# Performance work log

Hardware: AMD Instinct MI355X
Metric: run time of the kernel (lower is better)

The kernel has to match this reference:

```python
import jax, jax.numpy as jnp
import numpy as np

N_HEAD = 16

def setup_inputs() -> dict:
    key = jax.random.key(0)
    ks = jax.random.split(key, 5)
    C = 1024
    s = 1.0 / np.sqrt(C)
    x = jax.random.normal(ks[0], (2, 2048, C), dtype=jnp.float32)
    wq = jax.random.normal(ks[1], (C, C), dtype=jnp.float32) * s
    wk = jax.random.normal(ks[2], (C, C), dtype=jnp.float32) * s
    wv = jax.random.normal(ks[3], (C, C), dtype=jnp.float32) * s
    wp = jax.random.normal(ks[4], (C, C), dtype=jnp.float32) * s
    z = jnp.zeros((C,), dtype=jnp.float32)
    return {"x": x, "wq": wq, "bq": z, "wk": wk, "bk": z,
            "wv": wv, "bv": z, "wp": wp, "bp": z}

def reference(x, wq, bq, wk, bk, wv, bv, wp, bp):
    B, T, C = x.shape
    H = N_HEAD
    D = C // H
    # projections: weights stored as (in, out) -> x @ w + b
    q = (x @ wq + bq).reshape(B, T, H, D).transpose(0, 2, 1, 3)  # [B,H,T,D]
    k = (x @ wk + bk).reshape(B, T, H, D).transpose(0, 2, 1, 3)
    v = (x @ wv + bv).reshape(B, T, H, D).transpose(0, 2, 1, 3)
    att = jnp.einsum('bhqd,bhkd->bhqk', q, k) / jnp.sqrt(jnp.float32(D))
    causal = jnp.tril(jnp.ones((T, T), dtype=bool))
    att = jnp.where(causal[None, None], att, -jnp.inf)
    att = jax.nn.softmax(att, axis=-1)
    out = jnp.einsum('bhqk,bhkd->bhqd', att, v)  # [B,H,T,D]
    out = out.transpose(0, 2, 1, 3).reshape(B, T, C)
    return out @ wp + bp
```

## Files before the change

### kernel.cpp

```cpp
#include <hip/hip_runtime.h>
#include <hip/hip_bf16.h>
#include <stdint.h>


typedef __attribute__((ext_vector_type(8)))  short bf16x8;
typedef __attribute__((ext_vector_type(4)))  float f32x4;
typedef __attribute__((ext_vector_type(16))) float f32x16;
typedef __attribute__((ext_vector_type(4)))  short short4v;

#define MFMA16(a,b,c) __builtin_amdgcn_mfma_f32_16x16x32_bf16(a,b,c,0,0,0)
#define MFMA32(a,b,c) __builtin_amdgcn_mfma_f32_32x32x16_bf16(a,b,c,0,0,0)

__device__ __forceinline__ unsigned short f2bfu(float f){
  union { __hip_bfloat16 h; unsigned short u; } cv;
  cv.h = __float2bfloat16(f);
  return cv.u;
}

__device__ __forceinline__ unsigned cvtpk(float a, float b){
  unsigned r;
  asm("v_cvt_pk_bf16_f32 %0, %1, %2" : "=v"(r) : "v"(a), "v"(b));
  return r;
}

__device__ __forceinline__ void permswap(unsigned &x, unsigned &y){
  asm volatile("v_permlane32_swap_b32 %0, %1" : "+v"(x), "+v"(y));
}

__device__ __forceinline__ void async16(const void* g, void* s){
  __builtin_amdgcn_global_load_lds((const __attribute__((address_space(1))) void*)g,
                                   (__attribute__((address_space(3))) void*)s, 16, 0, 0);
}

__global__ __launch_bounds__(256)
void prep_k(const float* __restrict__ x, unsigned short* __restrict__ xb,
            const float* __restrict__ wq, const float* __restrict__ wk,
            const float* __restrict__ wv, const float* __restrict__ wp,
            unsigned short* __restrict__ wqkvT, unsigned short* __restrict__ wpT)
{
  __shared__ float t[32][33];
  const int bx = blockIdx.x;
  const int tid = threadIdx.x;
  if (bx < 4096) {
    const int i = bx * 256 + tid;
    const float4 v = ((const float4*)x)[i];
    short4v o;
    o.x = (short)f2bfu(v.x); o.y = (short)f2bfu(v.y);
    o.z = (short)f2bfu(v.z); o.w = (short)f2bfu(v.w);
    ((short4v*)xb)[i] = o;
    return;
  }
  const int b = bx - 4096;
  const int wsel = b >> 10;
  const float* W = (wsel == 0) ? wq : (wsel == 1) ? wk : (wsel == 2) ? wv : wp;
  unsigned short* Wt = (wsel == 3) ? wpT : wqkvT + (size_t)wsel * 1024 * 1024;
  const int bc = ((b & 1023) & 31) * 32;
  const int br = ((b & 1023) >> 5) * 32;
  const int tx = tid & 31, ty = tid >> 5;
  #pragma unroll
  for (int i = 0; i < 32; i += 8)
    t[ty + i][tx] = W[(size_t)(br + ty + i) * 1024 + bc + tx];
  __syncthreads();
  #pragma unroll
  for (int i = 0; i < 32; i += 8)
    Wt[(size_t)(bc + ty + i) * 1024 + br + tx] = f2bfu(t[tx][ty + i]);
}

template<int MODE>
__global__ __launch_bounds__(256)
void gemm_bt(const unsigned short* __restrict__ A, const unsigned short* __restrict__ Bt,
             const float* __restrict__ b0, const float* __restrict__ b1, const float* __restrict__ b2,
             unsigned short* __restrict__ Qo, unsigned short* __restrict__ Ko,
             unsigned short* __restrict__ Vo, float* __restrict__ Fo, int N)
{
  constexpr int K = 1024;
  __shared__ unsigned short As[2][128 * 32];
  __shared__ unsigned short Bs[2][128 * 32];
  const int tid = threadIdx.x;
  const int lane = tid & 63;
  const int w = tid >> 6;
  const int l15 = lane & 15, lhi = lane >> 4;
  const int row0 = blockIdx.y * 128;
  const int col0 = blockIdx.x * 128;
  const int wr = (w >> 1) * 64;
  const int wc = (w & 1) * 64;

  f32x4 acc[4][4];
  #pragma unroll
  for (int i = 0; i < 4; i++)
    #pragma unroll
    for (int j = 0; j < 4; j++) acc[i][j] = 0.0f;

  const int srow = lane >> 2;
  const int scol = (lane & 3) * 8;
  const unsigned short* Ab = A  + (size_t)(row0 + w * 32 + srow) * K + scol;
  const unsigned short* Bb = Bt + (size_t)(col0 + w * 32 + srow) * K + scol;
  const int wofs = (w * 32) * 32;

  auto stageg = [&](int k0, int buf) {
    async16(Ab + k0,          &As[buf][wofs]);
    async16(Ab + k0 + 16 * K, &As[buf][wofs + 16 * 32]);
    async16(Bb + k0,          &Bs[buf][wofs]);
    async16(Bb + k0 + 16 * K, &Bs[buf][wofs + 16 * 32]);
  };

  stageg(0, 0);
  __syncthreads();
  int cur = 0;
  for (int k0 = 0; k0 < K; k0 += 32) {
    if (k0 + 32 < K) stageg(k0 + 32, cur ^ 1);
    bf16x8 af[4], bfv[4];
    #pragma unroll
    for (int i = 0; i < 4; i++) {
      af[i]  = *(const bf16x8*)&As[cur][(wr + i * 16 + l15) * 32 + lhi * 8];
      bfv[i] = *(const bf16x8*)&Bs[cur][(wc + i * 16 + l15) * 32 + lhi * 8];
    }
    __builtin_amdgcn_s_setprio(1);
    #pragma unroll
    for (int i = 0; i < 4; i++)
      #pragma unroll
      for (int j = 0; j < 4; j++)
        acc[i][j] = MFMA16(af[i], bfv[j], acc[i][j]);
    __builtin_amdgcn_s_setprio(0);
    __syncthreads();
    cur ^= 1;
  }

  #pragma unroll
  for (int j = 0; j < 4; j++) {
    const int n = col0 + wc + j * 16 + l15;
    if constexpr (MODE == 0) {
      const int which = n >> 10;
      const int cn = n & 1023;
      const float bias = (which == 0 ? b0[cn] : which == 1 ? b1[cn] : b2[cn]);
      const int h = cn >> 6, d = cn & 63;
      if (which == 2) {
        #pragma unroll
        for (int i = 0; i < 4; i++) {
          const int m = row0 + wr + i * 16 + lhi * 4;
          const int b_ = m >> 11, t = m & 2047;
          uint2 pk;
          pk.x = cvtpk(acc[i][j][0] + bias, acc[i][j][1] + bias);
          pk.y = cvtpk(acc[i][j][2] + bias, acc[i][j][3] + bias);
          *(uint2*)(Vo + (((size_t)(b_ * 16 + h) * 64 + d) * 2048 + t)) = pk;
        }
      } else {
        unsigned short* dst = (which == 0 ? Qo : Ko);
        const float sc = (which == 0 ? 0.125f * 1.44269504f : 1.0f);
        #pragma unroll
        for (int i = 0; i < 4; i++)
          #pragma unroll
          for (int r = 0; r < 4; r++) {
            const int m = row0 + wr + i * 16 + lhi * 4 + r;
            const int b_ = m >> 11, t = m & 2047;
            dst[(((size_t)(b_ * 16 + h) * 2048 + t) * 64) + d] =
                f2bfu((acc[i][j][r] + bias) * sc);
          }
      }
    } else {
      const float bias = b0[n];
      #pragma unroll
      for (int i = 0; i < 4; i++)
        #pragma unroll
        for (int r = 0; r < 4; r++) {
          const int m = row0 + wr + i * 16 + lhi * 4 + r;
          Fo[(size_t)m * N + n] = acc[i][j][r] + bias;
        }
    }
  }
}


__global__ __launch_bounds__(256, 1)
void attn_k(const unsigned short* __restrict__ Q, const unsigned short* __restrict__ Kg,
            const unsigned short* __restrict__ VT, unsigned short* __restrict__ O)
{
  __shared__ unsigned short Ks[2][64 * 64];
  __shared__ unsigned short Vs[2][64 * 64];
  const int flat = blockIdx.y * 8 + blockIdx.x;
  const int u = (flat & 7) * 32 + (flat >> 3);
  const int bx = u & 7, bh = u >> 3;
  const int b_ = bh >> 4, h = bh & 15;
  const int tid = threadIdx.x, lane = tid & 63, w = tid >> 6;
  const int r0 = lane & 31, hi5 = lane >> 5;
  const int p  = bx * 4 + w;
  const int pB = 63 - p;
  const int q0A = p * 32, q0B = pB * 32;
  const int jmA = p >> 1, jmB = pB >> 1;
  const int jmax = (63 - bx * 4) >> 1;

  const unsigned short* Kbh  = Kg + (size_t)bh * (2048 * 64);
  const unsigned short* VTbh = VT + (size_t)bh * (64 * 2048);

  bf16x8 qfA[4], qfB[4];
  {
    const unsigned short* QA = Q + ((size_t)bh * 2048 + q0A + r0) * 64 + hi5 * 8;
    const unsigned short* QB = Q + ((size_t)bh * 2048 + q0B + r0) * 64 + hi5 * 8;
    #pragma unroll
    for (int s = 0; s < 4; s++) {
      qfA[s] = *(const bf16x8*)(QA + s * 16);
      qfB[s] = *(const bf16x8*)(QB + s * 16);
    }
  }

  f32x16 oA[2], oB[2];
  #pragma unroll
  for (int d = 0; d < 2; d++) { oA[d] = 0.0f; oB[d] = 0.0f; }
  float mA = -1e30f, lA = 0.0f, mB = -1e30f, lB = 0.0f;

  int fragoff[4];
  #pragma unroll
  for (int t = 0; t < 4; t++)
    fragoff[t] = (r0 * 128 + t * 32 + hi5 * 16) ^ ((r0 & 7) << 4);

  const int srow = w * 8 + (lane >> 3);
  const int cole = (((lane & 7) ^ (lane >> 3)) << 3);
  const unsigned short* Ksrc = Kbh + (size_t)srow * 64 + cole;
  const unsigned short* Vsrc = VTbh + (size_t)srow * 2048 + cole;

  auto stage = [&](int kv0, int buf) {
    unsigned short* kb = &Ks[buf][w * 512];
    unsigned short* vb = &Vs[buf][w * 512];
    #pragma unroll
    for (int it = 0; it < 2; ++it) {
      async16(Ksrc + (size_t)(kv0 + it * 32) * 64, kb + it * 2048);
      async16(Vsrc + (size_t)(it * 32) * 2048 + kv0, vb + it * 2048);
    }
  };

  const unsigned short* Ksb;
  const unsigned short* Vsb;

  auto member = [&](f32x16 (&oT)[2], const bf16x8 (&qf)[4],
                    float& mrun, float& lrun, int q0, int kv0, bool mask) {
    f32x16 s0 = 0.0f, s1 = 0.0f;
    __builtin_amdgcn_s_setprio(1);
    #pragma unroll
    for (int t = 0; t < 4; t++) {
      const bf16x8 ka = *(const bf16x8*)((const char*)Ksb + fragoff[t]);
      const bf16x8 kb = *(const bf16x8*)((const char*)Ksb + fragoff[t] + 4096);
      s0 = MFMA32(ka, qf[t], s0);
      s1 = MFMA32(kb, qf[t], s1);
    }
    __builtin_amdgcn_s_setprio(0);

    const int q = q0 + r0;
    if (mask) {
      #pragma unroll
      for (int r = 0; r < 16; r++) {
        const int kvr = kv0 + (r & 3) + 8 * (r >> 2) + 4 * hi5;
        if (kvr      > q) s0[r] = -1e30f;
        if (kvr + 32 > q) s1[r] = -1e30f;
      }
    }

    float pm = fmaxf(s0[0], s1[0]);
    #pragma unroll
    for (int r = 1; r < 16; r++) pm = fmaxf(pm, fmaxf(s0[r], s1[r]));
    pm = fmaxf(pm, __shfl_xor(pm, 32, 64));

    if (__any((int)(pm > mrun + 8.0f))) {
      const float mnew = fmaxf(mrun, pm);
      const float sc = exp2f(mrun - mnew);
      mrun = mnew; lrun *= sc;
      oT[0] *= sc; oT[1] *= sc;
    }

    float p0[16], p1[16];
    float rs = 0.0f;
    #pragma unroll
    for (int r = 0; r < 16; r++) {
      p0[r] = exp2f(s0[r] - mrun);
      p1[r] = exp2f(s1[r] - mrun);
      rs += p0[r] + p1[r];
    }
    rs += __shfl_xor(rs, 32, 64);
    lrun += rs;

    bf16x8 pb[4];
    #pragma unroll
    for (int sub = 0; sub < 2; sub++) {
      {
        unsigned a = cvtpk(p0[sub*8+0], p0[sub*8+1]);
        unsigned b = cvtpk(p0[sub*8+2], p0[sub*8+3]);
        unsigned c = cvtpk(p0[sub*8+4], p0[sub*8+5]);
        unsigned d = cvtpk(p0[sub*8+6], p0[sub*8+7]);
        permswap(a, c); permswap(b, d);
        union { unsigned u[4]; bf16x8 hv; } wv_;
        wv_.u[0] = a; wv_.u[1] = b; wv_.u[2] = c; wv_.u[3] = d;
        pb[sub] = wv_.hv;
      }
      {
        unsigned a = cvtpk(p1[sub*8+0], p1[sub*8+1]);
        unsigned b = cvtpk(p1[sub*8+2], p1[sub*8+3]);
        unsigned c = cvtpk(p1[sub*8+4], p1[sub*8+5]);
        unsigned d = cvtpk(p1[sub*8+6], p1[sub*8+7]);
        permswap(a, c); permswap(b, d);
        union { unsigned u[4]; bf16x8 hv; } wv_;
        wv_.u[0] = a; wv_.u[1] = b; wv_.u[2] = c; wv_.u[3] = d;
        pb[2 + sub] = wv_.hv;
      }
    }

    __builtin_amdgcn_s_setprio(1);
    #pragma unroll
    for (int t = 0; t < 4; t++) {
      const bf16x8 va = *(const bf16x8*)((const char*)Vsb + fragoff[t]);
      const bf16x8 vb = *(const bf16x8*)((const char*)Vsb + fragoff[t] + 4096);
      oT[0] = MFMA32(va, pb[t], oT[0]);
      oT[1] = MFMA32(vb, pb[t], oT[1]);
    }
    __builtin_amdgcn_s_setprio(0);
  };

  stage(0, 0);
  __syncthreads();

  int cur = 0;
  for (int j = 0; j <= jmax; ++j) {
    if (j < jmax) stage((j + 1) * 64, cur ^ 1);
    Ksb = &Ks[cur][0];
    Vsb = &Vs[cur][0];
    const int kv0 = j * 64;
    if (j <= jmB) member(oB, qfB, mB, lB, q0B, kv0, j == jmB);
    if (j <= jmA) member(oA, qfA, mA, lA, q0A, kv0, j == jmA);
    __syncthreads();
    cur ^= 1;
  }

  auto emit = [&](f32x16 (&oT)[2], float lr, int q0) {
    const float linv = 1.0f / lr;
    const int q = q0 + r0;
    unsigned short* obase = O + ((size_t)b_ * 2048 + q) * 1024 + h * 64 + hi5 * 4;
    #pragma unroll
    for (int dh = 0; dh < 2; dh++)
      #pragma unroll
      for (int g = 0; g < 4; g++) {
        uint2 pk;
        pk.x = cvtpk(oT[dh][4*g]   * linv, oT[dh][4*g+1] * linv);
        pk.y = cvtpk(oT[dh][4*g+2] * linv, oT[dh][4*g+3] * linv);
        *(uint2*)(obase + dh * 32 + g * 8) = pk;
      }
  };
  emit(oA, lA, q0A);
  emit(oB, lB, q0B);
}


extern "C" void kernel_launch(void* const* d_in, const int* in_sizes, int n_in,
                              void* d_out, int out_size, void* d_ws, size_t ws_size,
                              hipStream_t stream) {
  const float* x  = (const float*)d_in[0];
  const float* wq = (const float*)d_in[1];
  const float* bq = (const float*)d_in[2];
  const float* wk = (const float*)d_in[3];
  const float* bk = (const float*)d_in[4];
  const float* wv = (const float*)d_in[5];
  const float* bv = (const float*)d_in[6];
  const float* wp = (const float*)d_in[7];
  const float* bp = (const float*)d_in[8];
  float* out = (float*)d_out;

  char* ws = (char*)d_ws;
  const size_t MB = 1024 * 1024;
  unsigned short* xb    = (unsigned short*)(ws);
  unsigned short* wqkvT = (unsigned short*)(ws + 8  * MB);
  unsigned short* wpT   = (unsigned short*)(ws + 14 * MB);
  unsigned short* Qb    = (unsigned short*)(ws + 16 * MB);
  unsigned short* Kb    = (unsigned short*)(ws + 24 * MB);
  unsigned short* VTb   = (unsigned short*)(ws + 32 * MB);
  unsigned short* Ob    = (unsigned short*)(ws);

  prep_k<<<dim3(8192), dim3(256), 0, stream>>>(x, xb, wq, wk, wv, wp, wqkvT, wpT);

  gemm_bt<0><<<dim3(24, 32), dim3(256), 0, stream>>>(xb, wqkvT, bq, bk, bv,
                                                     Qb, Kb, VTb, nullptr, 3072);
  attn_k<<<dim3(8, 32), dim3(256), 0, stream>>>(Qb, Kb, VTb, Ob);
  gemm_bt<1><<<dim3(8, 32), dim3(256), 0, stream>>>(Ob, wpT, bp, nullptr, nullptr,
                                                    nullptr, nullptr, nullptr, out, 1024);
}
```

Baseline: 143.4 us.

## Split attention KV range across two blocks and merge partial outputs

The attention launch gains a grid z-dimension of 2. Each block processes alternating 64-wide KV tiles and writes a normalized partial output plus its per-row max and sum. A new combine kernel merges the two partials into the bf16 buffer used by the output projection. This doubles the attention block count and drops the min-blocks-per-CU launch bound, aiming for more concurrent work and better latency hiding per CU. The cost is an extra kernel launch, extra global traffic for the partials, and reuse of workspace and output memory as scratch.

Result: faster. 126.3 us (median of 2 runs) (-12.0%).

```diff
diff --git a/kernel.cpp b/kernel.cpp
--- a/kernel.cpp
+++ b/kernel.cpp
@@ -15,6 +15,11 @@
   union { __hip_bfloat16 h; unsigned short u; } cv;
   cv.h = __float2bfloat16(f);
   return cv.u;
+}
+__device__ __forceinline__ float bfu2f(unsigned u){
+  union { unsigned v; float f; } cv;
+  cv.v = u << 16;
+  return cv.f;
 }
 
 __device__ __forceinline__ unsigned cvtpk(float a, float b){
@@ -171,16 +176,18 @@
 }
 
 
-__global__ __launch_bounds__(256, 1)
+__global__ __launch_bounds__(256)
 void attn_k(const unsigned short* __restrict__ Q, const unsigned short* __restrict__ Kg,
-            const unsigned short* __restrict__ VT, unsigned short* __restrict__ O)
+            const unsigned short* __restrict__ VT,
+            unsigned short* __restrict__ Op0, unsigned short* __restrict__ Op1,
+            float* __restrict__ ml0, float* __restrict__ ml1)
 {
   __shared__ unsigned short Ks[2][64 * 64];
   __shared__ unsigned short Vs[2][64 * 64];
   const int flat = blockIdx.y * 8 + blockIdx.x;
   const int u = (flat & 7) * 32 + (flat >> 3);
   const int bx = u & 7, bh = u >> 3;
-  const int b_ = bh >> 4, h = bh & 15;
+  const int e = blockIdx.z;
   const int tid = threadIdx.x, lane = tid & 63, w = tid >> 6;
   const int r0 = lane & 31, hi5 = lane >> 5;
   const int p  = bx * 4 + w;
@@ -188,6 +195,9 @@
   const int q0A = p * 32, q0B = pB * 32;
   const int jmA = p >> 1, jmB = pB >> 1;
   const int jmax = (63 - bx * 4) >> 1;
+
+  unsigned short* Op = e ? Op1 : Op0;
+  float* ml = e ? ml1 : ml0;
 
   const unsigned short* Kbh  = Kg + (size_t)bh * (2048 * 64);
   const unsigned short* VTbh = VT + (size_t)bh * (64 * 2048);
@@ -313,37 +323,74 @@
     __builtin_amdgcn_s_setprio(0);
   };
 
-  stage(0, 0);
+  stage(e * 64, 0);
   __syncthreads();
 
   int cur = 0;
-  for (int j = 0; j <= jmax; ++j) {
-    if (j < jmax) stage((j + 1) * 64, cur ^ 1);
+  for (int t = e; t <= jmax; t += 2) {
+    if (t + 2 <= jmax) stage((t + 2) * 64, cur ^ 1);
     Ksb = &Ks[cur][0];
     Vsb = &Vs[cur][0];
-    const int kv0 = j * 64;
-    if (j <= jmB) member(oB, qfB, mB, lB, q0B, kv0, j == jmB);
-    if (j <= jmA) member(oA, qfA, mA, lA, q0A, kv0, j == jmA);
+    const int kv0 = t * 64;
+    if (t <= jmB) member(oB, qfB, mB, lB, q0B, kv0, t == jmB);
+    if (t <= jmA) member(oA, qfA, mA, lA, q0A, kv0, t == jmA);
     __syncthreads();
     cur ^= 1;
   }
 
-  auto emit = [&](f32x16 (&oT)[2], float lr, int q0) {
-    const float linv = 1.0f / lr;
-    const int q = q0 + r0;
-    unsigned short* obase = O + ((size_t)b_ * 2048 + q) * 1024 + h * 64 + hi5 * 4;
+  auto emitp = [&](f32x16 (&oT)[2], float m, float l, int p_) {
+    const float inv = (l > 0.0f) ? 1.0f / l : 0.0f;
+    const size_t rbase = (size_t)(bh * 64 + p_) * 32 + r0;
+    if (hi5 == 0) {
+      float2 v; v.x = m; v.y = l;
+      *(float2*)(ml + rbase * 2) = v;
+    }
+    unsigned short* base = Op + rbase * 64 + hi5 * 4;
     #pragma unroll
     for (int dh = 0; dh < 2; dh++)
       #pragma unroll
       for (int g = 0; g < 4; g++) {
         uint2 pk;
-        pk.x = cvtpk(oT[dh][4*g]   * linv, oT[dh][4*g+1] * linv);
-        pk.y = cvtpk(oT[dh][4*g+2] * linv, oT[dh][4*g+3] * linv);
-        *(uint2*)(obase + dh * 32 + g * 8) = pk;
+        pk.x = cvtpk(oT[dh][4*g]   * inv, oT[dh][4*g+1] * inv);
+        pk.y = cvtpk(oT[dh][4*g+2] * inv, oT[dh][4*g+3] * inv);
+        *(uint2*)(base + dh * 32 + g * 8) = pk;
       }
   };
-  emit(oA, lA, q0A);
-  emit(oB, lB, q0B);
+  emitp(oA, mA, lA, p);
+  emitp(oB, mB, lB, pB);
+}
+
+__global__ __launch_bounds__(256)
+void combine_k(const unsigned short* __restrict__ O0, const unsigned short* __restrict__ O1,
+               const float* __restrict__ ml0, const float* __restrict__ ml1,
+               unsigned short* __restrict__ Ob)
+{
+  const int g = blockIdx.x;
+  const int bh = g >> 6, p = g & 63;
+  const int b_ = bh >> 4, h = bh & 15;
+  const int tid = threadIdx.x;
+  const int row = tid >> 3, c8 = (tid & 7) * 8;
+  const size_t rbase = (size_t)g * 32 + row;
+  const float2 v0 = *(const float2*)(ml0 + rbase * 2);
+  const float2 v1 = *(const float2*)(ml1 + rbase * 2);
+  const float mm = fmaxf(v0.x, v1.x);
+  const float w0 = v0.y * exp2f(v0.x - mm);
+  const float w1 = v1.y * exp2f(v1.x - mm);
+  const float inv = 1.0f / (w0 + w1);
+  const float a0 = w0 * inv, a1 = w1 * inv;
+  const uint4 u0 = *(const uint4*)(O0 + rbase * 64 + c8);
+  const uint4 u1 = *(const uint4*)(O1 + rbase * 64 + c8);
+  uint4 o;
+  o.x = cvtpk(a0 * bfu2f(u0.x & 0xffffu) + a1 * bfu2f(u1.x & 0xffffu),
+              a0 * bfu2f(u0.x >> 16)     + a1 * bfu2f(u1.x >> 16));
+  o.y = cvtpk(a0 * bfu2f(u0.y & 0xffffu) + a1 * bfu2f(u1.y & 0xffffu),
+              a0 * bfu2f(u0.y >> 16)     + a1 * bfu2f(u1.y >> 16));
+  o.z = cvtpk(a0 * bfu2f(u0.z & 0xffffu) + a1 * bfu2f(u1.z & 0xffffu),
+              a0 * bfu2f(u0.z >> 16)     + a1 * bfu2f(u1.z >> 16));
+  o.w = cvtpk(a0 * bfu2f(u0.w & 0xffffu) + a1 * bfu2f(u1.w & 0xffffu),
+              a0 * bfu2f(u0.w >> 16)     + a1 * bfu2f(u1.w >> 16));
+  unsigned short* dst = Ob + ((size_t)b_ * 2048 + p * 32 + row) * 1024 + h * 64 + c8;
+  *(uint4*)dst = o;
 }
 
 
@@ -369,13 +416,18 @@
   unsigned short* Qb    = (unsigned short*)(ws + 16 * MB);
   unsigned short* Kb    = (unsigned short*)(ws + 24 * MB);
   unsigned short* VTb   = (unsigned short*)(ws + 32 * MB);
-  unsigned short* Ob    = (unsigned short*)(ws);
+  unsigned short* Op0   = (unsigned short*)(ws);
+  float*          ml0   = (float*)(ws + 8 * MB);
+  float*          ml1   = (float*)(ws + 8 * MB + 512 * 1024);
+  unsigned short* Op1   = (unsigned short*)d_out;
+  unsigned short* Ob    = Qb;
 
   prep_k<<<dim3(8192), dim3(256), 0, stream>>>(x, xb, wq, wk, wv, wp, wqkvT, wpT);
 
   gemm_bt<0><<<dim3(24, 32), dim3(256), 0, stream>>>(xb, wqkvT, bq, bk, bv,
                                                      Qb, Kb, VTb, nullptr, 3072);
-  attn_k<<<dim3(8, 32), dim3(256), 0, stream>>>(Qb, Kb, VTb, Ob);
+  attn_k<<<dim3(8, 32, 2), dim3(256), 0, stream>>>(Qb, Kb, VTb, Op0, Op1, ml0, ml1);
+  combine_k<<<dim3(2048), dim3(256), 0, stream>>>(Op0, Op1, ml0, ml1, Ob);
   gemm_bt<1><<<dim3(8, 32), dim3(256), 0, stream>>>(Ob, wpT, bp, nullptr, nullptr,
                                                     nullptr, nullptr, nullptr, out, 1024);
 }
```
